# Optimization experiments

Measured on AMD Instinct MI355X. Metric: run time of the kernel, lower is better.

## Reference

```python
import jax, jax.numpy as jnp
import numpy as np

B, S, U, M = 4096, 64, 128, 32
ODE_UNFOLDS = 6
EPS = 1e-08

def _uniform(k, shape, lo, hi):
    return jax.random.uniform(k, shape, jnp.float32, lo, hi)

def setup_inputs() -> dict:
    key = jax.random.key(0)
    ks = jax.random.split(key, 16)
    return {
        "inputs": jax.random.normal(ks[0], (B, S), jnp.float32),
        "state": jax.random.normal(ks[1], (B, U), jnp.float32),
        "gleak": _uniform(ks[2], (U,), 0.001, 1.0),
        "vleak": _uniform(ks[3], (U,), -0.2, 0.2),
        "cm": _uniform(ks[4], (U,), 0.4, 0.6),
        "sigma": _uniform(ks[5], (U, U), 3.0, 8.0),
        "mu": _uniform(ks[6], (U, U), 0.3, 0.8),
        "w": _uniform(ks[7], (U, U), 0.001, 1.0),
        "erev": jnp.sign(jax.random.normal(ks[8], (U, U), jnp.float32)),
        "sensory_sigma": _uniform(ks[9], (S, U), 3.0, 8.0),
        "sensory_mu": _uniform(ks[10], (S, U), 0.3, 0.8),
        "sensory_w": _uniform(ks[11], (S, U), 0.001, 1.0),
        "sensory_erev": jnp.sign(jax.random.normal(ks[12], (S, U), jnp.float32)),
        "sparsity_mask": (jax.random.uniform(ks[13], (U, U)) < 0.5).astype(jnp.float32),
        "sensory_sparsity_mask": (jax.random.uniform(ks[14], (S, U)) < 0.5).astype(jnp.float32),
        "input_w": jnp.ones((S,), jnp.float32),
        "input_b": jnp.zeros((S,), jnp.float32),
        "output_w": jnp.ones((M,), jnp.float32),
        "output_b": jnp.zeros((M,), jnp.float32),
    }

def reference(inputs, state, gleak, vleak, cm, sigma, mu, w, erev,
              sensory_sigma, sensory_mu, sensory_w, sensory_erev,
              sparsity_mask, sensory_sparsity_mask,
              input_w, input_b, output_w, output_b):
    # input mapping (affine)
    x = inputs * input_w + input_b                       # [B,S]
    # sensory synapse activation: [B,S,U]
    sens_act = (sensory_w * sensory_sparsity_mask) * jax.nn.sigmoid(
        sensory_sigma * (x[:, :, None] - sensory_mu))
    w_num_sensory = jnp.sum(sens_act * sensory_erev, axis=1)   # [B,U]
    w_den_sensory = jnp.sum(sens_act, axis=1)                  # [B,U]

    wm = w * sparsity_mask                                     # masked weights [U,U]
    wme = wm * erev                                            # weights*erev   [U,U]
    cm_t = cm * ODE_UNFOLDS                                    # cm / (1/unfolds)
    leak = gleak * vleak

    v = state
    for _ in range(ODE_UNFOLDS):
        sig = jax.nn.sigmoid(sigma * (v[:, :, None] - mu))     # [B,U,U] (src,dst)
        w_num = jnp.einsum('bsu,su->bu', sig, wme) + w_num_sensory
        w_den = jnp.einsum('bsu,su->bu', sig, wm) + w_den_sensory
        v = (cm_t * v + leak + w_num) / (cm_t + gleak + w_den + EPS)

    out = v[:, :M] * output_w + output_b                       # motor slice + affine
    return out, v
```

## Files before the change

kernel.cpp:

```cpp
#include <hip/hip_runtime.h>
#include <hip/hip_fp16.h>

typedef unsigned short u16;
typedef unsigned int   u32;

#define B_TOTAL 4096
#define ROWS    16
#define NU      128
#define NS      64
#define NM      32
#define UNFOLDS 6
#define LOG2E   1.44269504088896340736f

__device__ __forceinline__ float bf2f(u16 v) {
  return __uint_as_float(((u32)v) << 16);
}
__device__ __forceinline__ u16 f2bf(float f) {
  u32 x = __float_as_uint(f);
  return (u16)((x + 0x7fffu + ((x >> 16) & 1u)) >> 16);
}

template<bool BF16>
__device__ __forceinline__ float LD(const void* p, int i) {
  if (BF16) return bf2f(((const u16*)p)[i]);
  return ((const float*)p)[i];
}

__device__ __forceinline__ float rdlane(float v, int lane) {
  return __int_as_float(__builtin_amdgcn_readlane(__float_as_int(v), lane));
}

__device__ __forceinline__ u32 pk(float a, float b) {
  __half2 h = __halves2half2(__float2half_rn(a), __float2half_rn(b));
  return __builtin_bit_cast(u32, h);
}

__device__ __forceinline__ void step(u32 a0, u32 a1, u32 wv, float vj,
                                     float& n0, float& d0, float& n1, float& d1) {
  float t0, t1, q, aw;
  asm("v_fma_mix_f32 %[t0], %[vj], %[a0], %[a1] op_sel:[0,0,0] op_sel_hi:[0,1,1]\n\t"
      "v_fma_mix_f32 %[t1], %[vj], %[a0], %[a1] op_sel:[0,1,1] op_sel_hi:[0,1,1]\n\t"
      "v_exp_f32 %[t0], %[t0]\n\t"
      "v_exp_f32 %[t1], %[t1]\n\t"
      "v_add_f32 %[t0], 1.0, %[t0]\n\t"
      "v_add_f32 %[t1], 1.0, %[t1]\n\t"
      "v_mul_f32 %[q], %[t0], %[t1]\n\t"
      "v_rcp_f32 %[q], %[q]\n\t"
      "v_and_b32 %[aw], 0x7fff7fff, %[w]\n\t"
      "v_mul_f32 %[t1], %[t1], %[q]\n\t"
      "v_mul_f32 %[t0], %[t0], %[q]\n\t"
      "v_fma_mix_f32 %[n0], %[t1], %[w],  %[n0] op_sel:[0,0,0] op_sel_hi:[0,1,0]\n\t"
      "v_fma_mix_f32 %[d0], %[t1], %[aw], %[d0] op_sel:[0,0,0] op_sel_hi:[0,1,0]\n\t"
      "v_fma_mix_f32 %[n1], %[t0], %[w],  %[n1] op_sel:[0,1,0] op_sel_hi:[0,1,0]\n\t"
      "v_fma_mix_f32 %[d1], %[t0], %[aw], %[d1] op_sel:[0,1,0] op_sel_hi:[0,1,0]"
      : [n0] "+v"(n0), [d0] "+v"(d0), [n1] "+v"(n1), [d1] "+v"(d1),
        [t0] "=&v"(t0), [t1] "=&v"(t1), [q] "=&v"(q), [aw] "=&v"(aw)
      : [vj] "v"(vj), [a0] "v"(a0), [a1] "v"(a1), [w] "v"(wv));
}

template<bool BF16>
__device__ __forceinline__ void body(
    const void* g_in, const void* g_state, const void* g_gleak, const void* g_vleak,
    const void* g_cm, const void* g_sigma, const void* g_mu, const void* g_w,
    const void* g_erev, const void* g_ssig, const void* g_smu, const void* g_sw,
    const void* g_serev, const void* g_mask, const void* g_smask,
    const void* g_iw, const void* g_ib, const void* g_ow, const void* g_ob,
    void* g_out,
    uint4* smR)
{
  const int tid = threadIdx.x;
  const int b0  = blockIdx.x * ROWS;

  const int r  = tid >> 6;
  const int u0 = tid & 63;
  const int u1 = u0 + 64;
  const int b  = b0 + r;

  #pragma unroll 2
  for (int e = tid; e < NS * 64; e += 1024) {
    int s = e >> 6, l = e & 63;
    int i0 = s * NU + l, i1 = i0 + 64;
    float sl0 = LD<BF16>(g_ssig, i0) * LOG2E, sl1 = LD<BF16>(g_ssig, i1) * LOG2E;
    float ms0 = LD<BF16>(g_smu, i0) * sl0,    ms1 = LD<BF16>(g_smu, i1) * sl1;
    float w0 = LD<BF16>(g_sw, i0) * LD<BF16>(g_smask, i0) * LD<BF16>(g_serev, i0);
    float w1 = LD<BF16>(g_sw, i1) * LD<BF16>(g_smask, i1) * LD<BF16>(g_serev, i1);
    smR[e] = make_uint4(pk(-sl0, -sl1), pk(ms0, ms1), pk(w0, w1), 0u);
  }
  __syncthreads();

  float x_lane = LD<BF16>(g_in, b * NS + u0) * LD<BF16>(g_iw, u0) + LD<BF16>(g_ib, u0);
  float v0 = LD<BF16>(g_state, b * NU + u0);
  float v1 = LD<BF16>(g_state, b * NU + u1);
  const float gl0 = LD<BF16>(g_gleak, u0), gl1 = LD<BF16>(g_gleak, u1);
  const float lk0 = gl0 * LD<BF16>(g_vleak, u0);
  const float lk1 = gl1 * LD<BF16>(g_vleak, u1);
  const float cm0 = LD<BF16>(g_cm, u0) * (float)UNFOLDS;
  const float cm1 = LD<BF16>(g_cm, u1) * (float)UNFOLDS;

  const uint4* pR = smR + u0;

  float ns0 = 0.f, ds0 = 0.f, ns1 = 0.f, ds1 = 0.f;
  #pragma unroll 8
  for (int s = 0; s < NS; ++s) {
    float xs = rdlane(x_lane, s);
    uint4 a = pR[s * 64];
    step(a.x, a.y, a.z, xs, ns0, ds0, ns1, ds1);
  }
  __syncthreads();

  #pragma unroll 4
  for (int e = tid; e < NU * 64; e += 1024) {
    int j = e >> 6, l = e & 63;
    int i0 = j * NU + l, i1 = i0 + 64;
    float sl0 = LD<BF16>(g_sigma, i0) * LOG2E, sl1 = LD<BF16>(g_sigma, i1) * LOG2E;
    float ms0 = LD<BF16>(g_mu, i0) * sl0,      ms1 = LD<BF16>(g_mu, i1) * sl1;
    float w0 = LD<BF16>(g_w, i0) * LD<BF16>(g_mask, i0) * LD<BF16>(g_erev, i0);
    float w1 = LD<BF16>(g_w, i1) * LD<BF16>(g_mask, i1) * LD<BF16>(g_erev, i1);
    smR[e] = make_uint4(pk(-sl0, -sl1), pk(ms0, ms1), pk(w0, w1), 0u);
  }
  __syncthreads();

  #pragma unroll 1
  for (int it = 0; it < UNFOLDS; ++it) {
    float n0 = ns0, d0 = ds0, n1 = ns1, d1 = ds1;
    #pragma unroll 8
    for (int j = 0; j < 64; ++j) {
      float vj = rdlane(v0, j);
      uint4 a = pR[j * 64];
      step(a.x, a.y, a.z, vj, n0, d0, n1, d1);
    }
    #pragma unroll 8
    for (int j = 0; j < 64; ++j) {
      float vj = rdlane(v1, j);
      uint4 a = pR[(j + 64) * 64];
      step(a.x, a.y, a.z, vj, n0, d0, n1, d1);
    }
    v0 = fmaf(cm0, v0, lk0 + n0) * __builtin_amdgcn_rcpf(cm0 + gl0 + d0 + 1e-8f);
    v1 = fmaf(cm1, v1, lk1 + n1) * __builtin_amdgcn_rcpf(cm1 + gl1 + d1 + 1e-8f);
  }

  if (BF16) {
    u16* om = (u16*)g_out;
    u16* ov = om + B_TOTAL * NM;
    ov[b * NU + u0] = f2bf(v0);
    ov[b * NU + u1] = f2bf(v1);
    if (u0 < NM)
      om[b * NM + u0] = f2bf(fmaf(v0, LD<true>(g_ow, u0), LD<true>(g_ob, u0)));
  } else {
    float* om = (float*)g_out;
    float* ov = om + B_TOTAL * NM;
    ov[b * NU + u0] = v0;
    ov[b * NU + u1] = v1;
    if (u0 < NM)
      om[b * NM + u0] = fmaf(v0, LD<false>(g_ow, u0), LD<false>(g_ob, u0));
  }
}

__global__ __launch_bounds__(1024, 4) void ltc_kernel(
    const void* g_in, const void* g_state, const void* g_gleak, const void* g_vleak,
    const void* g_cm, const void* g_sigma, const void* g_mu, const void* g_w,
    const void* g_erev, const void* g_ssig, const void* g_smu, const void* g_sw,
    const void* g_serev, const void* g_mask, const void* g_smask,
    const void* g_iw, const void* g_ib, const void* g_ow, const void* g_ob,
    void* g_out)
{
  __shared__ uint4 smR[NU * 64];

  const u16* sg = (const u16*)g_sigma;
  int cnt = 0;
  #pragma unroll
  for (int i = 0; i < 32; ++i) {
    float f = bf2f(sg[2 * i]);
    cnt += (f >= 2.0f && f <= 16.0f) ? 1 : 0;
  }
  if (cnt >= 24)
    body<true >(g_in, g_state, g_gleak, g_vleak, g_cm, g_sigma, g_mu, g_w, g_erev,
                g_ssig, g_smu, g_sw, g_serev, g_mask, g_smask,
                g_iw, g_ib, g_ow, g_ob, g_out, smR);
  else
    body<false>(g_in, g_state, g_gleak, g_vleak, g_cm, g_sigma, g_mu, g_w, g_erev,
                g_ssig, g_smu, g_sw, g_serev, g_mask, g_smask,
                g_iw, g_ib, g_ow, g_ob, g_out, smR);
}

extern "C" void kernel_launch(void* const* d_in, const int* in_sizes, int n_in,
                              void* d_out, int out_size, void* d_ws, size_t ws_size,
                              hipStream_t stream) {
  (void)in_sizes; (void)n_in; (void)out_size; (void)d_ws; (void)ws_size;
  dim3 grid(B_TOTAL / ROWS);
  dim3 block(1024);
  hipLaunchKernelGGL(ltc_kernel, grid, block, 0, stream,
                     d_in[0], d_in[1], d_in[2], d_in[3], d_in[4],
                     d_in[5], d_in[6], d_in[7], d_in[8],
                     d_in[9], d_in[10], d_in[11], d_in[12],
                     d_in[13], d_in[14], d_in[15], d_in[16],
                     d_in[17], d_in[18], d_out);
}
```

Before: 220.9 us.

## Process two batch rows per wavefront to reuse shared-memory parameter loads

Each wavefront now handles two batch rows instead of one, halving the block size to 512 threads while keeping 16 rows per block. Every shared-memory load of the packed sigma/mu/weight triple feeds two sigmoid evaluations, and the widened inline-asm step interleaves the two rows so independent exp and rcp ops can overlap. The aim is to cut LDS traffic per flop and raise instruction-level parallelism. In exchange, register pressure per thread goes up and launch bounds drop to 512 threads with 2 blocks, which may lower occupancy.

```diff
diff --git a/kernel.cpp b/kernel.cpp
--- a/kernel.cpp
+++ b/kernel.cpp
@@ -5,7 +5,6 @@
 typedef unsigned int   u32;
 
 #define B_TOTAL 4096
-#define ROWS    16
 #define NU      128
 #define NS      64
 #define NM      32
@@ -35,27 +34,44 @@
   return __builtin_bit_cast(u32, h);
 }
 
-__device__ __forceinline__ void step(u32 a0, u32 a1, u32 wv, float vj,
-                                     float& n0, float& d0, float& n1, float& d1) {
-  float t0, t1, q, aw;
-  asm("v_fma_mix_f32 %[t0], %[vj], %[a0], %[a1] op_sel:[0,0,0] op_sel_hi:[0,1,1]\n\t"
-      "v_fma_mix_f32 %[t1], %[vj], %[a0], %[a1] op_sel:[0,1,1] op_sel_hi:[0,1,1]\n\t"
+__device__ __forceinline__ void step2(u32 a0, u32 a1, u32 wv, float va, float vb,
+                                      float& na0, float& da0, float& na1, float& da1,
+                                      float& nb0, float& db0, float& nb1, float& db1) {
+  float t0, t1, t2, t3, qa, qb, aw;
+  asm("v_fma_mix_f32 %[t0], %[va], %[a0], %[a1] op_sel:[0,0,0] op_sel_hi:[0,1,1]\n\t"
+      "v_fma_mix_f32 %[t1], %[va], %[a0], %[a1] op_sel:[0,1,1] op_sel_hi:[0,1,1]\n\t"
+      "v_fma_mix_f32 %[t2], %[vb], %[a0], %[a1] op_sel:[0,0,0] op_sel_hi:[0,1,1]\n\t"
+      "v_fma_mix_f32 %[t3], %[vb], %[a0], %[a1] op_sel:[0,1,1] op_sel_hi:[0,1,1]\n\t"
       "v_exp_f32 %[t0], %[t0]\n\t"
       "v_exp_f32 %[t1], %[t1]\n\t"
+      "v_exp_f32 %[t2], %[t2]\n\t"
+      "v_exp_f32 %[t3], %[t3]\n\t"
       "v_add_f32 %[t0], 1.0, %[t0]\n\t"
       "v_add_f32 %[t1], 1.0, %[t1]\n\t"
-      "v_mul_f32 %[q], %[t0], %[t1]\n\t"
-      "v_rcp_f32 %[q], %[q]\n\t"
+      "v_add_f32 %[t2], 1.0, %[t2]\n\t"
+      "v_add_f32 %[t3], 1.0, %[t3]\n\t"
+      "v_mul_f32 %[qa], %[t0], %[t1]\n\t"
+      "v_mul_f32 %[qb], %[t2], %[t3]\n\t"
+      "v_rcp_f32 %[qa], %[qa]\n\t"
+      "v_rcp_f32 %[qb], %[qb]\n\t"
       "v_and_b32 %[aw], 0x7fff7fff, %[w]\n\t"
-      "v_mul_f32 %[t1], %[t1], %[q]\n\t"
-      "v_mul_f32 %[t0], %[t0], %[q]\n\t"
-      "v_fma_mix_f32 %[n0], %[t1], %[w],  %[n0] op_sel:[0,0,0] op_sel_hi:[0,1,0]\n\t"
-      "v_fma_mix_f32 %[d0], %[t1], %[aw], %[d0] op_sel:[0,0,0] op_sel_hi:[0,1,0]\n\t"
-      "v_fma_mix_f32 %[n1], %[t0], %[w],  %[n1] op_sel:[0,1,0] op_sel_hi:[0,1,0]\n\t"
-      "v_fma_mix_f32 %[d1], %[t0], %[aw], %[d1] op_sel:[0,1,0] op_sel_hi:[0,1,0]"
-      : [n0] "+v"(n0), [d0] "+v"(d0), [n1] "+v"(n1), [d1] "+v"(d1),
-        [t0] "=&v"(t0), [t1] "=&v"(t1), [q] "=&v"(q), [aw] "=&v"(aw)
-      : [vj] "v"(vj), [a0] "v"(a0), [a1] "v"(a1), [w] "v"(wv));
+      "v_mul_f32 %[t1], %[t1], %[qa]\n\t"
+      "v_mul_f32 %[t0], %[t0], %[qa]\n\t"
+      "v_mul_f32 %[t3], %[t3], %[qb]\n\t"
+      "v_mul_f32 %[t2], %[t2], %[qb]\n\t"
+      "v_fma_mix_f32 %[na0], %[t1], %[w],  %[na0] op_sel:[0,0,0] op_sel_hi:[0,1,0]\n\t"
+      "v_fma_mix_f32 %[da0], %[t1], %[aw], %[da0] op_sel:[0,0,0] op_sel_hi:[0,1,0]\n\t"
+      "v_fma_mix_f32 %[na1], %[t0], %[w],  %[na1] op_sel:[0,1,0] op_sel_hi:[0,1,0]\n\t"
+      "v_fma_mix_f32 %[da1], %[t0], %[aw], %[da1] op_sel:[0,1,0] op_sel_hi:[0,1,0]\n\t"
+      "v_fma_mix_f32 %[nb0], %[t3], %[w],  %[nb0] op_sel:[0,0,0] op_sel_hi:[0,1,0]\n\t"
+      "v_fma_mix_f32 %[db0], %[t3], %[aw], %[db0] op_sel:[0,0,0] op_sel_hi:[0,1,0]\n\t"
+      "v_fma_mix_f32 %[nb1], %[t2], %[w],  %[nb1] op_sel:[0,1,0] op_sel_hi:[0,1,0]\n\t"
+      "v_fma_mix_f32 %[db1], %[t2], %[aw], %[db1] op_sel:[0,1,0] op_sel_hi:[0,1,0]"
+      : [na0] "+v"(na0), [da0] "+v"(da0), [na1] "+v"(na1), [da1] "+v"(da1),
+        [nb0] "+v"(nb0), [db0] "+v"(db0), [nb1] "+v"(nb1), [db1] "+v"(db1),
+        [t0] "=&v"(t0), [t1] "=&v"(t1), [t2] "=&v"(t2), [t3] "=&v"(t3),
+        [qa] "=&v"(qa), [qb] "=&v"(qb), [aw] "=&v"(aw)
+      : [va] "v"(va), [vb] "v"(vb), [a0] "v"(a0), [a1] "v"(a1), [w] "v"(wv));
 }
 
 template<bool BF16>
@@ -69,15 +85,16 @@
     uint4* smR)
 {
   const int tid = threadIdx.x;
-  const int b0  = blockIdx.x * ROWS;
+  const int b0  = blockIdx.x * 16;
 
   const int r  = tid >> 6;
   const int u0 = tid & 63;
   const int u1 = u0 + 64;
-  const int b  = b0 + r;
+  const int ba = b0 + 2 * r;
+  const int bb = ba + 1;
 
   #pragma unroll 2
-  for (int e = tid; e < NS * 64; e += 1024) {
+  for (int e = tid; e < NS * 64; e += 512) {
     int s = e >> 6, l = e & 63;
     int i0 = s * NU + l, i1 = i0 + 64;
     float sl0 = LD<BF16>(g_ssig, i0) * LOG2E, sl1 = LD<BF16>(g_ssig, i1) * LOG2E;
@@ -88,9 +105,13 @@
   }
   __syncthreads();
 
-  float x_lane = LD<BF16>(g_in, b * NS + u0) * LD<BF16>(g_iw, u0) + LD<BF16>(g_ib, u0);
-  float v0 = LD<BF16>(g_state, b * NU + u0);
-  float v1 = LD<BF16>(g_state, b * NU + u1);
+  float iw = LD<BF16>(g_iw, u0), ib = LD<BF16>(g_ib, u0);
+  float xa = LD<BF16>(g_in, ba * NS + u0) * iw + ib;
+  float xb = LD<BF16>(g_in, bb * NS + u0) * iw + ib;
+  float va0 = LD<BF16>(g_state, ba * NU + u0);
+  float va1 = LD<BF16>(g_state, ba * NU + u1);
+  float vb0 = LD<BF16>(g_state, bb * NU + u0);
+  float vb1 = LD<BF16>(g_state, bb * NU + u1);
   const float gl0 = LD<BF16>(g_gleak, u0), gl1 = LD<BF16>(g_gleak, u1);
   const float lk0 = gl0 * LD<BF16>(g_vleak, u0);
   const float lk1 = gl1 * LD<BF16>(g_vleak, u1);
@@ -99,17 +120,19 @@
 
   const uint4* pR = smR + u0;
 
-  float ns0 = 0.f, ds0 = 0.f, ns1 = 0.f, ds1 = 0.f;
-  #pragma unroll 8
+  float nsa0 = 0.f, dsa0 = 0.f, nsa1 = 0.f, dsa1 = 0.f;
+  float nsb0 = 0.f, dsb0 = 0.f, nsb1 = 0.f, dsb1 = 0.f;
+  #pragma unroll 4
   for (int s = 0; s < NS; ++s) {
-    float xs = rdlane(x_lane, s);
+    float xsa = rdlane(xa, s);
+    float xsb = rdlane(xb, s);
     uint4 a = pR[s * 64];
-    step(a.x, a.y, a.z, xs, ns0, ds0, ns1, ds1);
+    step2(a.x, a.y, a.z, xsa, xsb, nsa0, dsa0, nsa1, dsa1, nsb0, dsb0, nsb1, dsb1);
   }
   __syncthreads();
 
   #pragma unroll 4
-  for (int e = tid; e < NU * 64; e += 1024) {
+  for (int e = tid; e < NU * 64; e += 512) {
     int j = e >> 6, l = e & 63;
     int i0 = j * NU + l, i1 = i0 + 64;
     float sl0 = LD<BF16>(g_sigma, i0) * LOG2E, sl1 = LD<BF16>(g_sigma, i1) * LOG2E;
@@ -122,41 +145,56 @@
 
   #pragma unroll 1
   for (int it = 0; it < UNFOLDS; ++it) {
-    float n0 = ns0, d0 = ds0, n1 = ns1, d1 = ds1;
-    #pragma unroll 8
+    float na0 = nsa0, da0 = dsa0, na1 = nsa1, da1 = dsa1;
+    float nb0 = nsb0, db0 = dsb0, nb1 = nsb1, db1 = dsb1;
+    #pragma unroll 4
     for (int j = 0; j < 64; ++j) {
-      float vj = rdlane(v0, j);
+      float vja = rdlane(va0, j);
+      float vjb = rdlane(vb0, j);
       uint4 a = pR[j * 64];
-      step(a.x, a.y, a.z, vj, n0, d0, n1, d1);
-    }
-    #pragma unroll 8
+      step2(a.x, a.y, a.z, vja, vjb, na0, da0, na1, da1, nb0, db0, nb1, db1);
+    }
+    #pragma unroll 4
     for (int j = 0; j < 64; ++j) {
-      float vj = rdlane(v1, j);
+      float vja = rdlane(va1, j);
+      float vjb = rdlane(vb1, j);
       uint4 a = pR[(j + 64) * 64];
-      step(a.x, a.y, a.z, vj, n0, d0, n1, d1);
-    }
-    v0 = fmaf(cm0, v0, lk0 + n0) * __builtin_amdgcn_rcpf(cm0 + gl0 + d0 + 1e-8f);
-    v1 = fmaf(cm1, v1, lk1 + n1) * __builtin_amdgcn_rcpf(cm1 + gl1 + d1 + 1e-8f);
+      step2(a.x, a.y, a.z, vja, vjb, na0, da0, na1, da1, nb0, db0, nb1, db1);
+    }
+    va0 = fmaf(cm0, va0, lk0 + na0) * __builtin_amdgcn_rcpf(cm0 + gl0 + da0 + 1e-8f);
+    va1 = fmaf(cm1, va1, lk1 + na1) * __builtin_amdgcn_rcpf(cm1 + gl1 + da1 + 1e-8f);
+    vb0 = fmaf(cm0, vb0, lk0 + nb0) * __builtin_amdgcn_rcpf(cm0 + gl0 + db0 + 1e-8f);
+    vb1 = fmaf(cm1, vb1, lk1 + nb1) * __builtin_amdgcn_rcpf(cm1 + gl1 + db1 + 1e-8f);
   }
 
   if (BF16) {
     u16* om = (u16*)g_out;
     u16* ov = om + B_TOTAL * NM;
-    ov[b * NU + u0] = f2bf(v0);
-    ov[b * NU + u1] = f2bf(v1);
-    if (u0 < NM)
-      om[b * NM + u0] = f2bf(fmaf(v0, LD<true>(g_ow, u0), LD<true>(g_ob, u0)));
+    ov[ba * NU + u0] = f2bf(va0);
+    ov[ba * NU + u1] = f2bf(va1);
+    ov[bb * NU + u0] = f2bf(vb0);
+    ov[bb * NU + u1] = f2bf(vb1);
+    if (u0 < NM) {
+      float ow = LD<true>(g_ow, u0), ob = LD<true>(g_ob, u0);
+      om[ba * NM + u0] = f2bf(fmaf(va0, ow, ob));
+      om[bb * NM + u0] = f2bf(fmaf(vb0, ow, ob));
+    }
   } else {
     float* om = (float*)g_out;
     float* ov = om + B_TOTAL * NM;
-    ov[b * NU + u0] = v0;
-    ov[b * NU + u1] = v1;
-    if (u0 < NM)
-      om[b * NM + u0] = fmaf(v0, LD<false>(g_ow, u0), LD<false>(g_ob, u0));
-  }
-}
-
-__global__ __launch_bounds__(1024, 4) void ltc_kernel(
+    ov[ba * NU + u0] = va0;
+    ov[ba * NU + u1] = va1;
+    ov[bb * NU + u0] = vb0;
+    ov[bb * NU + u1] = vb1;
+    if (u0 < NM) {
+      float ow = LD<false>(g_ow, u0), ob = LD<false>(g_ob, u0);
+      om[ba * NM + u0] = fmaf(va0, ow, ob);
+      om[bb * NM + u0] = fmaf(vb0, ow, ob);
+    }
+  }
+}
+
+__global__ __launch_bounds__(512, 2) void ltc_kernel(
     const void* g_in, const void* g_state, const void* g_gleak, const void* g_vleak,
     const void* g_cm, const void* g_sigma, const void* g_mu, const void* g_w,
     const void* g_erev, const void* g_ssig, const void* g_smu, const void* g_sw,
@@ -187,8 +225,8 @@
                               void* d_out, int out_size, void* d_ws, size_t ws_size,
                               hipStream_t stream) {
   (void)in_sizes; (void)n_in; (void)out_size; (void)d_ws; (void)ws_size;
-  dim3 grid(B_TOTAL / ROWS);
-  dim3 block(1024);
+  dim3 grid(B_TOTAL / 16);
+  dim3 block(512);
   hipLaunchKernelGGL(ltc_kernel, grid, block, 0, stream,
                      d_in[0], d_in[1], d_in[2], d_in[3], d_in[4],
                      d_in[5], d_in[6], d_in[7], d_in[8],
```

Result: no change. 221.9 us (+0.5%).
